# Performance work log

Hardware: AMD Instinct MI355X
Metric: run time of the kernel (lower is better)

## Reference

```python
import jax, jax.numpy as jnp
import numpy as np

VOCAB = 30000
K1 = 1.2
B_PARAM = 0.75


def setup_inputs() -> dict:
    key = jax.random.key(0)
    k1, k2 = jax.random.split(key)
    B, L = 2048, 512
    input_ids = jax.random.randint(k1, (B, L), 0, VOCAB, dtype=jnp.int64)
    attention_mask = jnp.ones((B, L), dtype=jnp.int64)
    W = jax.random.normal(k2, (768, VOCAB), dtype=jnp.float32) / np.sqrt(VOCAB)
    return {"input_ids": input_ids, "attention_mask": attention_mask, "W": W}


def reference(input_ids, attention_mask, W):
    B, L = input_ids.shape
    # valid tokens: attended AND 100 < id < VOCAB
    valid = (attention_mask == 1) & (input_ids > 100) & (input_ids < VOCAB)
    validf = valid.astype(jnp.float32)
    doc_len = validf.sum(-1)  # [B]

    # batched histogram (TF counts) via scatter-add; invalid entries add 0 at slot 0
    rows = jnp.broadcast_to(jnp.arange(B)[:, None], (B, L))
    toks = jnp.where(valid, input_ids, 0)
    tf = jnp.zeros((B, VOCAB), jnp.float32).at[rows, toks].add(validf)  # [B, VOCAB]

    # BM25 scoring; torch writes scores only at unique tokens -> equivalent to masking tf>0
    length_norm = jnp.maximum(1.0 + B_PARAM * (doc_len / 100.0 - 1.0), 0.5)[:, None]
    scores = jnp.where(tf > 0, tf * (K1 + 1.0) / (tf + K1 * length_norm), 0.0)

    v = scores + 1e-10
    v = v / jnp.linalg.norm(v, axis=-1, keepdims=True)  # F.normalize p=2

    out = v @ W.T  # Linear(VOCAB, 768, bias=False)
    out = out / jnp.linalg.norm(out, axis=-1, keepdims=True)
    return out
```

## Files before the change

### kernel.cpp

```cpp
#include <hip/hip_runtime.h>
#include <hip/hip_bf16.h>
#include <stdint.h>

#define B_ROWS 2048
#define SEQ 512
#define VOC 30000
#define DMODEL 768
#define K1 1.2f
#define BPAR 0.75f
#define NT 192
#define PF 8

__global__ void transpose_W(const float* __restrict__ W, __hip_bfloat16* __restrict__ Wb) {
    __shared__ float tile[32][33];
    int tBase = blockIdx.x * 32;
    int jBase = blockIdx.y * 32;
    int tx = threadIdx.x, ty = threadIdx.y;
#pragma unroll
    for (int k = 0; k < 4; k++) {
        int j = jBase + ty + k * 8;
        int t = tBase + tx;
        float v = (t < VOC) ? W[(size_t)j * VOC + t] : 0.f;
        tile[ty + k * 8][tx] = v;
    }
    __syncthreads();
#pragma unroll
    for (int k = 0; k < 4; k++) {
        int t = tBase + ty + k * 8;
        if (t < VOC) Wb[(size_t)t * DMODEL + jBase + tx] = __float2bfloat16(tile[tx][ty + k * 8]);
    }
}

__device__ __forceinline__ float b2f(unsigned short h) {
    union { uint32_t u; float f; } v; v.u = ((uint32_t)h) << 16; return v.f;
}

__launch_bounds__(NT, 6)
__global__ void bm25_main(const int* __restrict__ ids, const int* __restrict__ mask,
                          const __hip_bfloat16* __restrict__ Wb,
                          float* __restrict__ out) {
    __shared__ int   stoks[SEQ];
    __shared__ uint2 tw[SEQ];
    __shared__ int   nv;
    __shared__ float wred[3];

    int b = blockIdx.x;
    int tid = threadIdx.x;
    const char* __restrict__ Wbase = (const char*)Wb;
    uint32_t tid8 = (uint32_t)tid << 3;

    if (tid == 0) nv = 0;
    __syncthreads();

    for (int i = tid; i < SEQ; i += NT) {
        int id = ids[(size_t)b * SEQ + i];
        int m  = mask[(size_t)b * SEQ + i];
        if (m == 1 && id > 100 && id < VOC) {
            stoks[atomicAdd(&nv, 1)] = id;
        }
    }
    __syncthreads();
    int n = nv;

    for (int i = n + tid; i < SEQ; i += NT) stoks[i] = 0x7fffffff;

    for (int k = 2; k <= SEQ; k <<= 1) {
        for (int j = k >> 1; j > 0; j >>= 1) {
            __syncthreads();
            for (int i = tid; i < SEQ; i += NT) {
                int ixj = i ^ j;
                if (ixj > i) {
                    int a = stoks[i], c = stoks[ixj];
                    if ((a > c) == ((i & k) == 0)) { stoks[i] = c; stoks[ixj] = a; }
                }
            }
        }
    }
    __syncthreads();

    float kln = K1 * fmaxf(1.0f + BPAR * ((float)n / 100.0f - 1.0f), 0.5f);
    for (int i = tid; i < n; i += NT) {
        int t = stoks[i];
        int lo = i; while (lo > 0 && stoks[lo - 1] == t) lo--;
        int hi = i; while (hi < n - 1 && stoks[hi + 1] == t) hi++;
        float w = (K1 + 1.0f) / ((float)(hi - lo + 1) + kln);
        tw[i] = make_uint2((uint32_t)t * (DMODEL * 2u), __float_as_uint(w));
    }
    __syncthreads();

#define LOADB(R, WV, P)                                                        \
    _Pragma("unroll")                                                          \
    for (int q = 0; q < PF; q++) {                                             \
        uint2 t_ = tw[(P) + q];                                                \
        (R)[q] = *(const ushort4*)(Wbase + (t_.x + tid8));                     \
        (WV)[q] = __uint_as_float(t_.y);                                       \
    }
#define FMAB(R, WV)                                                            \
    _Pragma("unroll")                                                          \
    for (int q = 0; q < PF; q++) {                                             \
        acc.x = fmaf((WV)[q], b2f((R)[q].x), acc.x);                           \
        acc.y = fmaf((WV)[q], b2f((R)[q].y), acc.y);                           \
        acc.z = fmaf((WV)[q], b2f((R)[q].z), acc.z);                           \
        acc.w = fmaf((WV)[q], b2f((R)[q].w), acc.w);                           \
    }

    float4 acc = make_float4(0.f, 0.f, 0.f, 0.f);
    int nfull = n & ~(PF - 1);
    if (nfull) {
        ushort4 cur[PF]; float wcur[PF];
        LOADB(cur, wcur, 0)
        for (int p = PF; p < nfull; p += PF) {
            ushort4 nxt[PF]; float wnxt[PF];
            LOADB(nxt, wnxt, p)
            FMAB(cur, wcur)
#pragma unroll
            for (int q = 0; q < PF; q++) { cur[q] = nxt[q]; wcur[q] = wnxt[q]; }
        }
        FMAB(cur, wcur)
    }
    for (int p = nfull; p < n; p++) {
        uint2 t_ = tw[p];
        float w = __uint_as_float(t_.y);
        ushort4 r = *(const ushort4*)(Wbase + (t_.x + tid8));
        acc.x = fmaf(w, b2f(r.x), acc.x);
        acc.y = fmaf(w, b2f(r.y), acc.y);
        acc.z = fmaf(w, b2f(r.z), acc.z);
        acc.w = fmaf(w, b2f(r.w), acc.w);
    }

    float ss = acc.x * acc.x + acc.y * acc.y + acc.z * acc.z + acc.w * acc.w;
#pragma unroll
    for (int off = 32; off > 0; off >>= 1) ss += __shfl_down(ss, off);
    if ((tid & 63) == 0) wred[tid >> 6] = ss;
    __syncthreads();
    float inv = rsqrtf(fmaxf(wred[0] + wred[1] + wred[2], 1e-30f));

    float4 o;
    o.x = acc.x * inv; o.y = acc.y * inv; o.z = acc.z * inv; o.w = acc.w * inv;
    ((float4*)(out + (size_t)b * DMODEL))[tid] = o;
}

extern "C" void kernel_launch(void* const* d_in, const int* in_sizes, int n_in,
                              void* d_out, int out_size, void* d_ws, size_t ws_size,
                              hipStream_t stream) {
    const int*   ids  = (const int*)d_in[0];
    const int*   mask = (const int*)d_in[1];
    const float* W    = (const float*)d_in[2];
    float* out = (float*)d_out;

    __hip_bfloat16* Wb = (__hip_bfloat16*)d_ws;

    dim3 tgrid((VOC + 31) / 32, DMODEL / 32);
    dim3 tblock(32, 8);
    transpose_W<<<tgrid, tblock, 0, stream>>>(W, Wb);

    bm25_main<<<B_ROWS, NT, 0, stream>>>(ids, mask, Wb, out);
}
```

Baseline: 177.1 us.

## Split token gather across two thread groups with 16-byte row loads

The block's 192 threads now form two groups of 96. Each thread loads 8 bf16 columns (16 bytes) per token instead of 4, and the two groups handle alternate tokens. Partial accumulators are reduced through shared memory before the norm and the store. The aim is fewer, wider global loads and two independent token streams, at the cost of an extra reduction step, more shared memory, and dropping the old software prefetch pipeline.

After: 239.7 us. 1.35x slower.

```diff
diff --git a/kernel.cpp b/kernel.cpp
--- a/kernel.cpp
+++ b/kernel.cpp
@@ -9,6 +9,7 @@
 #define K1 1.2f
 #define BPAR 0.75f
 #define NT 192
+#define GSZ 96
 #define PF 8
 
 __global__ void transpose_W(const float* __restrict__ W, __hip_bfloat16* __restrict__ Wb) {
@@ -31,8 +32,15 @@
     }
 }
 
-__device__ __forceinline__ float b2f(unsigned short h) {
-    union { uint32_t u; float f; } v; v.u = ((uint32_t)h) << 16; return v.f;
+__device__ __forceinline__ void fma8(float* a, const uint4& r, float w) {
+    a[0] = fmaf(w, __uint_as_float(r.x << 16), a[0]);
+    a[1] = fmaf(w, __uint_as_float(r.x & 0xffff0000u), a[1]);
+    a[2] = fmaf(w, __uint_as_float(r.y << 16), a[2]);
+    a[3] = fmaf(w, __uint_as_float(r.y & 0xffff0000u), a[3]);
+    a[4] = fmaf(w, __uint_as_float(r.z << 16), a[4]);
+    a[5] = fmaf(w, __uint_as_float(r.z & 0xffff0000u), a[5]);
+    a[6] = fmaf(w, __uint_as_float(r.w << 16), a[6]);
+    a[7] = fmaf(w, __uint_as_float(r.w & 0xffff0000u), a[7]);
 }
 
 __launch_bounds__(NT, 6)
@@ -42,12 +50,16 @@
     __shared__ int   stoks[SEQ];
     __shared__ uint2 tw[SEQ];
     __shared__ int   nv;
-    __shared__ float wred[3];
+    __shared__ float accred[DMODEL];
+    __shared__ float ssbuf[GSZ];
+    __shared__ float wred;
 
     int b = blockIdx.x;
     int tid = threadIdx.x;
     const char* __restrict__ Wbase = (const char*)Wb;
-    uint32_t tid8 = (uint32_t)tid << 3;
+    int g = tid / GSZ;
+    int lane = tid - g * GSZ;
+    uint32_t col16 = (uint32_t)lane << 4;
 
     if (tid == 0) nv = 0;
     __syncthreads();
@@ -88,56 +100,56 @@
     }
     __syncthreads();
 
-#define LOADB(R, WV, P)                                                        \
-    _Pragma("unroll")                                                          \
-    for (int q = 0; q < PF; q++) {                                             \
-        uint2 t_ = tw[(P) + q];                                                \
-        (R)[q] = *(const ushort4*)(Wbase + (t_.x + tid8));                     \
-        (WV)[q] = __uint_as_float(t_.y);                                       \
+    float a[8] = {0.f, 0.f, 0.f, 0.f, 0.f, 0.f, 0.f, 0.f};
+    int m = (n + 1 - g) >> 1;
+    int mfull = m & ~(PF - 1);
+    for (int i0 = 0; i0 < mfull; i0 += PF) {
+        uint4 r[PF]; float w[PF];
+#pragma unroll
+        for (int q = 0; q < PF; q++) {
+            uint2 t_ = tw[((i0 + q) << 1) | g];
+            r[q] = *(const uint4*)(Wbase + (t_.x + col16));
+            w[q] = __uint_as_float(t_.y);
+        }
+#pragma unroll
+        for (int q = 0; q < PF; q++) fma8(a, r[q], w[q]);
     }
-#define FMAB(R, WV)                                                            \
-    _Pragma("unroll")                                                          \
-    for (int q = 0; q < PF; q++) {                                             \
-        acc.x = fmaf((WV)[q], b2f((R)[q].x), acc.x);                           \
-        acc.y = fmaf((WV)[q], b2f((R)[q].y), acc.y);                           \
-        acc.z = fmaf((WV)[q], b2f((R)[q].z), acc.z);                           \
-        acc.w = fmaf((WV)[q], b2f((R)[q].w), acc.w);                           \
+    for (int i = mfull; i < m; i++) {
+        uint2 t_ = tw[(i << 1) | g];
+        uint4 r = *(const uint4*)(Wbase + (t_.x + col16));
+        fma8(a, r, __uint_as_float(t_.y));
     }
 
-    float4 acc = make_float4(0.f, 0.f, 0.f, 0.f);
-    int nfull = n & ~(PF - 1);
-    if (nfull) {
-        ushort4 cur[PF]; float wcur[PF];
-        LOADB(cur, wcur, 0)
-        for (int p = PF; p < nfull; p += PF) {
-            ushort4 nxt[PF]; float wnxt[PF];
-            LOADB(nxt, wnxt, p)
-            FMAB(cur, wcur)
+    if (g == 1) {
+        ((float4*)accred)[lane * 2]     = make_float4(a[0], a[1], a[2], a[3]);
+        ((float4*)accred)[lane * 2 + 1] = make_float4(a[4], a[5], a[6], a[7]);
+    }
+    __syncthreads();
+    if (g == 0) {
+        float4 p0 = ((float4*)accred)[lane * 2];
+        float4 p1 = ((float4*)accred)[lane * 2 + 1];
+        a[0] += p0.x; a[1] += p0.y; a[2] += p0.z; a[3] += p0.w;
+        a[4] += p1.x; a[5] += p1.y; a[6] += p1.z; a[7] += p1.w;
+        float ss = 0.f;
 #pragma unroll
-            for (int q = 0; q < PF; q++) { cur[q] = nxt[q]; wcur[q] = wnxt[q]; }
-        }
-        FMAB(cur, wcur)
+        for (int d = 0; d < 8; d++) ss = fmaf(a[d], a[d], ss);
+        ssbuf[lane] = ss;
     }
-    for (int p = nfull; p < n; p++) {
-        uint2 t_ = tw[p];
-        float w = __uint_as_float(t_.y);
-        ushort4 r = *(const ushort4*)(Wbase + (t_.x + tid8));
-        acc.x = fmaf(w, b2f(r.x), acc.x);
-        acc.y = fmaf(w, b2f(r.y), acc.y);
-        acc.z = fmaf(w, b2f(r.z), acc.z);
-        acc.w = fmaf(w, b2f(r.w), acc.w);
+    __syncthreads();
+    if (tid < 64) {
+        float s = ssbuf[tid] + (tid < 32 ? ssbuf[tid + 64] : 0.f);
+#pragma unroll
+        for (int off = 32; off > 0; off >>= 1) s += __shfl_down(s, off);
+        if (tid == 0) wred = s;
     }
+    __syncthreads();
 
-    float ss = acc.x * acc.x + acc.y * acc.y + acc.z * acc.z + acc.w * acc.w;
-#pragma unroll
-    for (int off = 32; off > 0; off >>= 1) ss += __shfl_down(ss, off);
-    if ((tid & 63) == 0) wred[tid >> 6] = ss;
-    __syncthreads();
-    float inv = rsqrtf(fmaxf(wred[0] + wred[1] + wred[2], 1e-30f));
-
-    float4 o;
-    o.x = acc.x * inv; o.y = acc.y * inv; o.z = acc.z * inv; o.w = acc.w * inv;
-    ((float4*)(out + (size_t)b * DMODEL))[tid] = o;
+    if (g == 0) {
+        float inv = rsqrtf(fmaxf(wred, 1e-30f));
+        float4* outp = (float4*)(out + (size_t)b * DMODEL + lane * 8);
+        outp[0] = make_float4(a[0] * inv, a[1] * inv, a[2] * inv, a[3] * inv);
+        outp[1] = make_float4(a[4] * inv, a[5] * inv, a[6] * inv, a[7] * inv);
+    }
 }
 
 extern "C" void kernel_launch(void* const* d_in, const int* in_sizes, int n_in,
```
